# Kernel tuning notes

Measured on AMD Instinct MI355X. Metric: run time of the kernel, lower is better.

The kernel has to match this reference:

```python
import jax, jax.numpy as jnp
import numpy as np

E, B, T, DIN, D = 8, 16, 512, 256, 256  # ensemble, batch, seq, input_dim, d_model*factor


def setup_inputs() -> dict:
    key = jax.random.key(0)
    ks = jax.random.split(key, 9)
    s_in = 1.0 / np.sqrt(DIN)
    s_d = 1.0 / np.sqrt(D)
    return {
        "x": jax.random.normal(ks[0], (E, B, T, DIN), jnp.float32),
        "hidden": jnp.zeros((1, E * B, 2 * D), jnp.float32),
        "rnn_start": (jax.random.uniform(ks[1], (B, T, 1)) < 0.02).astype(jnp.float32),
        "W_in": jax.random.normal(ks[2], (2, E, DIN, D), jnp.float32) * s_in,
        "b_in": jax.random.normal(ks[3], (2, E, D), jnp.float32) * 0.01,
        "W_mid": jax.random.normal(ks[4], (4, E, D, D), jnp.float32) * s_d,
        "b_mid": jax.random.normal(ks[5], (4, E, D), jnp.float32) * 0.01,
        "W_out": jax.random.normal(ks[6], (E, D, D), jnp.float32) * s_d,
        "b_out": jax.random.normal(ks[7], (E, D), jnp.float32) * 0.01,
    }


def _scan_tie_input_gate(v, f, h0):
    # h_t = f_t * h_{t-1} + (1 - f_t) * v_t  (tied input gate), via associative scan.
    # v, f: [N, T, D]; h0: [N, 1, D]
    b = (1.0 - f) * v

    def combine(x, y):
        a1, b1 = x
        a2, b2 = y
        return a1 * a2, a2 * b1 + b2

    A, Bc = jax.lax.associative_scan(combine, (f, b), axis=1)
    out = A * h0 + Bc  # [N, T, D]
    return out, out[:, -1:, :]


def reference(x, hidden, rnn_start, W_in, b_in, W_mid, b_mid, W_out, b_out):
    # --- first GILR stage ---
    u = jnp.einsum('ebti,meio->mebto', x, W_in) + b_in[:, :, None, None, :]
    v = jnp.tanh(u[0])
    f = jax.nn.sigmoid(u[1])
    f = f * (1.0 - rnn_start)[None]  # rnn_start [B,T,1] broadcasts over E, D

    vr = v.reshape(E * B, T, D)
    fr = f.reshape(E * B, T, D)

    h_pre, h_mid = jnp.split(hidden, 2, axis=-1)          # each [1, E*B, D]
    h_pre = jnp.transpose(h_pre, (1, 0, 2))               # [E*B, 1, D]
    h_mid = jnp.transpose(h_mid, (1, 0, 2))

    vr, h_pre_last = _scan_tie_input_gate(vr, fr, h_pre)
    v4 = vr.reshape(E, B, T, D)

    # --- LSTM-like middle stage ---
    u = jnp.einsum('ebti,meio->mebto', v4, W_mid) + b_mid[:, :, None, None, :]
    f = jax.nn.sigmoid(u[0])
    i = jax.nn.sigmoid(u[1])
    o = jax.nn.sigmoid(u[2])
    z = jnp.tanh(u[3])
    f = f * (1.0 - rnn_start)[None]

    fr = f.reshape(E * B, T, D)
    izr = (i * z).reshape(E * B, T, D)
    orr = o.reshape(E * B, T, D)

    out, h_mid_last = _scan_tie_input_gate(izr, fr, h_mid)
    out = out * orr
    out4 = out.reshape(E, B, T, D)

    # --- output projection ---
    out4 = jnp.einsum('ebti,eio->ebto', out4, W_out) + b_out[:, None, None, :]

    hidden_out = jnp.transpose(jnp.concatenate([h_pre_last, h_mid_last], axis=-1), (1, 0, 2))
    return out4, hidden_out
```

## Files before the change

kernel.cpp:

```cpp
#include <hip/hip_runtime.h>
#include <hip/hip_bf16.h>
#include <stdint.h>
#include <stddef.h>


typedef __bf16 bf16x8 __attribute__((ext_vector_type(8)));
typedef __bf16 bf16x4 __attribute__((ext_vector_type(4)));
typedef __bf16 bf16x2 __attribute__((ext_vector_type(2)));
typedef float  f32x4  __attribute__((ext_vector_type(4)));
typedef unsigned int u32x2 __attribute__((ext_vector_type(2)));

#define E_ 8
#define M_ 8192
#define K_ 256

__device__ __forceinline__ float sigm_f(float x) {
    return __builtin_amdgcn_rcpf(1.0f + __expf(-x));
}
__device__ __forceinline__ float tanh_f(float x) {
    return 1.0f - 2.0f * __builtin_amdgcn_rcpf(1.0f + __expf(2.0f * x));
}

__device__ __forceinline__ void g2lds16(const void* g, void* l) {
    __builtin_amdgcn_global_load_lds((const __attribute__((address_space(1))) void*)g,
                                     (__attribute__((address_space(3))) void*)l, 16, 0, 0);
}

template <int D>
__device__ __forceinline__ float dppshr(float x) {
    return __builtin_bit_cast(float,
        __builtin_amdgcn_update_dpp(0, __builtin_bit_cast(int, x),
                                    0x110 | D, 0xF, 0xF, true));
}

__device__ __forceinline__ void lane_scan(float& A, float& B, float& EA, float& EB, int ln15) {
    float As, Bs;
    Bs = dppshr<1>(B); As = dppshr<1>(A); B = __builtin_fmaf(A, Bs, B); A = (ln15 >= 1) ? A * As : A;
    Bs = dppshr<2>(B); As = dppshr<2>(A); B = __builtin_fmaf(A, Bs, B); A = (ln15 >= 2) ? A * As : A;
    Bs = dppshr<4>(B); As = dppshr<4>(A); B = __builtin_fmaf(A, Bs, B); A = (ln15 >= 4) ? A * As : A;
    Bs = dppshr<8>(B); As = dppshr<8>(A); B = __builtin_fmaf(A, Bs, B); A = (ln15 >= 8) ? A * As : A;
    EA = dppshr<1>(A); EA = (ln15 >= 1) ? EA : 1.0f;
    EB = dppshr<1>(B);
}

__global__ __launch_bounds__(256) void convx_k(const float* __restrict__ x, __bf16* __restrict__ xb) {
    int i = blockIdx.x * 256 + threadIdx.x;
    float4 v = ((const float4*)x)[i];
    bf16x4 o;
    o[0] = (__bf16)v.x; o[1] = (__bf16)v.y; o[2] = (__bf16)v.z; o[3] = (__bf16)v.w;
    ((bf16x4*)xb)[i] = o;
}

__global__ __launch_bounds__(256) void transw_k(const float* __restrict__ src, __bf16* __restrict__ dst,
                                                int NG, int ilv) {
    int ge = blockIdx.z;
    int g = ge >> 3, e = ge & 7;
    int k0 = blockIdx.x * 64, d0 = blockIdx.y * 64;
    __shared__ float tile[64][65];
    int t = threadIdx.x;
#pragma unroll
    for (int j = 0; j < 16; ++j) {
        int lin = j * 256 + t;
        int r = lin >> 6, c = lin & 63;
        tile[r][c] = src[((size_t)(ge * 256 + k0 + r)) * 256 + d0 + c];
    }
    __syncthreads();
#pragma unroll
    for (int j = 0; j < 16; ++j) {
        int lin = j * 256 + t;
        int r = lin >> 6, c = lin & 63;
        int d = d0 + r;
        int row = ilv ? (d * NG + g) : (g * 256 + d);
        dst[((size_t)(e * NG * 256 + row)) * K_ + k0 + c] = (__bf16)tile[c][r];
    }
}

template <int MODE, int NG>
__global__ __launch_bounds__(512, 1) void gemm_k(const __bf16* __restrict__ A,
                                                 const __bf16* __restrict__ Wt,
                                                 const float* __restrict__ bias,
                                                 const float* __restrict__ rs,
                                                 __bf16* __restrict__ gout,
                                                 float* __restrict__ fout,
                                                 const float* __restrict__ hidden,
                                                 float* __restrict__ hidout) {
    constexpr int NT  = NG * 2;
    constexpr int NMT = 2 * NT;
    const int tid = threadIdx.x;
    const int bid = blockIdx.x;
    const int e  = bid & 7;
    const int rr = bid >> 3;
    const int nt = rr & (NT - 1);
    const int ms = rr / NT;
    const int mt0 = ms * NMT;
    const int lane = tid & 63, wid = tid >> 6;
    const int wr = wid >> 2, wc = wid & 3;
    const int ln15 = lane & 15, ln16 = lane >> 4;

    __shared__ __align__(16) __bf16 As[2][32768];
    __shared__ float cAl[64], cBl[64];
    __shared__ float chL[2][64];

    bf16x8 Breg[2][8];
    {
        const __bf16* bp = Wt + ((size_t)e * (NG * 256) + nt * 128 + wc * 32 + ln15) * K_ + ln16 * 8;
#pragma unroll
        for (int j = 0; j < 2; ++j)
#pragma unroll
            for (int s = 0; s < 8; ++s)
                Breg[j][s] = *(const bf16x8*)(bp + (size_t)j * 16 * K_ + s * 32);
    }
    f32x4 bias_v[2];
#pragma unroll
    for (int j = 0; j < 2; ++j) {
        int n0 = nt * 128 + wc * 32 + j * 16 + (ln16 << 2);
        if constexpr (MODE == 0) {
#pragma unroll
            for (int q = 0; q < 4; ++q) {
                int n = n0 + q;
                bias_v[j][q] = bias[((n & 1) * E_ + e) * 256 + (n >> 1)];
            }
        } else if constexpr (MODE == 1) {
#pragma unroll
            for (int q = 0; q < 4; ++q) {
                int n = n0 + q;
                bias_v[j][q] = bias[((n & 3) * E_ + e) * 256 + (n >> 2)];
            }
        } else {
            bias_v[j] = *(const f32x4*)&bias[e * 256 + n0];
        }
    }

    const size_t Ae = ((size_t)e * M_ + (size_t)mt0 * 128) * K_;
    const int sr = tid >> 5, sr2 = sr >> 2;
    const int gg0 = (tid & 31) ^ sr2;
    const __bf16* sE = A + Ae + (size_t)sr * K_ + gg0 * 8;
    const __bf16* sO = A + Ae + (size_t)sr * K_ + (gg0 ^ 4) * 8;
    __bf16* const dbase0 = &As[0][tid * 8];
    __bf16* const dbase1 = &As[1][tid * 8];

    auto stage = [&](int tt, int buf) {
        __bf16* d = buf ? dbase1 : dbase0;
        const size_t toff = (size_t)tt * (128 * K_);
#pragma unroll
        for (int q = 0; q < 8; ++q)
            g2lds16(((q & 1) ? sO : sE) + toff + q * (16 * K_), d + q * 4096);
    };

    const int rowb = (wr * 64 + ln15 * 4) * K_;
    const int gb = ln16 ^ (lane & 7);
    const int pe_off = rowb + gb * 8;
    const int po_off = rowb + (gb ^ 4) * 8;

    f32x4 acc[4][2] = {};

    auto compute = [&](int buf) {
        const __bf16* pe = &As[0][0] + buf * 32768 + pe_off;
        const __bf16* po = &As[0][0] + buf * 32768 + po_off;
#pragma unroll
        for (int s = 0; s < 8; ++s) {
            const __bf16* p = (s & 1) ? po : pe;
            bf16x8 af[4];
#pragma unroll
            for (int i = 0; i < 4; ++i)
                af[i] = *(const bf16x8*)(p + i * K_ + (s >> 1) * 64);
#pragma unroll
            for (int i = 0; i < 4; ++i)
#pragma unroll
                for (int j = 0; j < 2; ++j)
                    acc[i][j] = __builtin_amdgcn_mfma_f32_16x16x32_bf16(Breg[j][s], af[i], acc[i][j], 0, 0, 0);
        }
    };

    stage(0, 0);
    asm volatile("s_waitcnt vmcnt(0)" ::: "memory");
    __builtin_amdgcn_s_barrier();
    __builtin_amdgcn_sched_barrier(0);

    int buf = 0;
    for (int t = 0; t < NMT; ++t) {
        if (t + 1 < NMT) stage(t + 1, buf ^ 1);
        compute(buf);

        const int mt = mt0 + t;
        const int mb = mt * 128 + wr * 64 + ln15 * 4;

        if constexpr (MODE == 2) {
#pragma unroll
            for (int j = 0; j < 2; ++j) {
                const int n0 = nt * 128 + wc * 32 + j * 16 + (ln16 << 2);
#pragma unroll
                for (int i = 0; i < 4; ++i) {
                    f32x4 o = acc[i][j] + bias_v[j];
                    *(f32x4*)&fout[((size_t)e * M_ + mb + i) * 256 + n0] = o;
                    acc[i][j] = f32x4{};
                }
            }
        } else {
            f32x4 rs4 = *(const f32x4*)&rs[mb];
            f32x4 rsv;
#pragma unroll
            for (int q = 0; q < 4; ++q) rsv[q] = 1.0f - rs4[q];
            const bool cs = ((t & 3) == 0);
            const int c = t >> 2;

            if constexpr (MODE == 1) {
                float PA[2][4], PB[2][4], Ov[2][4], LA[2], LB[2], EA[2], EB[2];
#pragma unroll
                for (int j = 0; j < 2; ++j) {
#pragma unroll
                    for (int i = 0; i < 4; ++i) {
                        float f  = sigm_f(acc[i][j][0] + bias_v[j][0]) * rsv[i];
                        float iv = sigm_f(acc[i][j][1] + bias_v[j][1]);
                        float o  = sigm_f(acc[i][j][2] + bias_v[j][2]);
                        float z  = tanh_f(acc[i][j][3] + bias_v[j][3]);
                        float b  = (1.0f - f) * iv * z;
                        Ov[j][i] = o;
                        if (i == 0) { PA[j][0] = f; PB[j][0] = b; }
                        else { PB[j][i] = __builtin_fmaf(f, PB[j][i - 1], b); PA[j][i] = PA[j][i - 1] * f; }
                        acc[i][j] = f32x4{};
                    }
                    LA[j] = PA[j][3]; LB[j] = PB[j][3];
                    lane_scan(LA[j], LB[j], EA[j], EB[j], ln15);
                }
                if (wr == 0 && ln15 == 15) {
#pragma unroll
                    for (int j = 0; j < 2; ++j) {
                        int sl = wc * 8 + j * 4 + ln16;
                        cAl[sl] = LA[j]; cBl[sl] = LB[j];
                    }
                }
                asm volatile("s_waitcnt lgkmcnt(0)" ::: "memory");
                __builtin_amdgcn_s_barrier();
#pragma unroll
                for (int j = 0; j < 2; ++j) {
                    const int sl = wc * 8 + j * 4 + ln16;
                    const int d = nt * 32 + wc * 8 + j * 4 + ln16;
                    float hp = cs ? hidden[(e * 16 + ms * 4 + c) * 512 + 256 + d]
                                  : chL[t & 1][sl];
                    float hs = wr ? __builtin_fmaf(cAl[sl], hp, cBl[sl]) : hp;
                    float h0 = __builtin_fmaf(EA[j], hs, EB[j]);
#pragma unroll
                    for (int i = 0; i < 4; ++i) {
                        float h = __builtin_fmaf(PA[j][i], h0, PB[j][i]);
                        gout[((size_t)e * M_ + mb + i) * 256 + d] = (__bf16)(h * Ov[j][i]);
                    }
                    if (wr == 1 && ln15 == 15) {
                        float he = __builtin_fmaf(LA[j], hs, LB[j]);
                        chL[(t + 1) & 1][sl] = he;
                        if ((t & 3) == 3)
                            hidout[(e * 16 + ms * 4 + c) * 512 + 256 + d] = he;
                    }
                }
            } else {
                float PA[2][2][4], PB[2][2][4], LA[2][2], LB[2][2], EA[2][2], EB[2][2];
#pragma unroll
                for (int j = 0; j < 2; ++j) {
#pragma unroll
                    for (int dq = 0; dq < 2; ++dq) {
#pragma unroll
                        for (int i = 0; i < 4; ++i) {
                            float uv = acc[i][j][dq * 2 + 0] + bias_v[j][dq * 2 + 0];
                            float uf = acc[i][j][dq * 2 + 1] + bias_v[j][dq * 2 + 1];
                            float f = sigm_f(uf) * rsv[i];
                            float b = (1.0f - f) * tanh_f(uv);
                            if (i == 0) { PA[j][dq][0] = f; PB[j][dq][0] = b; }
                            else { PB[j][dq][i] = __builtin_fmaf(f, PB[j][dq][i - 1], b);
                                   PA[j][dq][i] = PA[j][dq][i - 1] * f; }
                        }
                        LA[j][dq] = PA[j][dq][3]; LB[j][dq] = PB[j][dq][3];
                        lane_scan(LA[j][dq], LB[j][dq], EA[j][dq], EB[j][dq], ln15);
                    }
#pragma unroll
                    for (int i = 0; i < 4; ++i) acc[i][j] = f32x4{};
                }
                if (wr == 0 && ln15 == 15) {
#pragma unroll
                    for (int j = 0; j < 2; ++j)
#pragma unroll
                        for (int dq = 0; dq < 2; ++dq) {
                            int sl = wc * 16 + j * 8 + ln16 * 2 + dq;
                            cAl[sl] = LA[j][dq]; cBl[sl] = LB[j][dq];
                        }
                }
                asm volatile("s_waitcnt lgkmcnt(0)" ::: "memory");
                __builtin_amdgcn_s_barrier();
#pragma unroll
                for (int j = 0; j < 2; ++j) {
                    const int D0 = nt * 64 + wc * 16 + j * 8 + ln16 * 2;
                    float h0q[2];
#pragma unroll
                    for (int dq = 0; dq < 2; ++dq) {
                        const int sl = wc * 16 + j * 8 + ln16 * 2 + dq;
                        float hp = cs ? hidden[(e * 16 + ms * 2 + c) * 512 + D0 + dq]
                                      : chL[t & 1][sl];
                        float hs = wr ? __builtin_fmaf(cAl[sl], hp, cBl[sl]) : hp;
                        h0q[dq] = __builtin_fmaf(EA[j][dq], hs, EB[j][dq]);
                        if (wr == 1 && ln15 == 15) {
                            float he = __builtin_fmaf(LA[j][dq], hs, LB[j][dq]);
                            chL[(t + 1) & 1][sl] = he;
                            if ((t & 3) == 3)
                                hidout[(e * 16 + ms * 2 + c) * 512 + D0 + dq] = he;
                        }
                    }
#pragma unroll
                    for (int i = 0; i < 4; ++i) {
                        float ha = __builtin_fmaf(PA[j][0][i], h0q[0], PB[j][0][i]);
                        float hb = __builtin_fmaf(PA[j][1][i], h0q[1], PB[j][1][i]);
                        bf16x2 pk; pk[0] = (__bf16)ha; pk[1] = (__bf16)hb;
                        *(unsigned int*)&gout[((size_t)e * M_ + mb + i) * 256 + D0] =
                            __builtin_bit_cast(unsigned int, pk);
                    }
                }
            }
        }
        asm volatile("s_waitcnt vmcnt(8) lgkmcnt(0)" ::: "memory");
        __builtin_amdgcn_s_barrier();
        __builtin_amdgcn_sched_barrier(0);
        buf ^= 1;
    }
}

extern "C" void kernel_launch(void* const* d_in, const int* in_sizes, int n_in,
                              void* d_out, int out_size, void* d_ws, size_t ws_size,
                              hipStream_t stream) {
    const float* x      = (const float*)d_in[0];
    const float* hidden = (const float*)d_in[1];
    const float* rs     = (const float*)d_in[2];
    const float* W_in   = (const float*)d_in[3];
    const float* b_in   = (const float*)d_in[4];
    const float* W_mid  = (const float*)d_in[5];
    const float* b_mid  = (const float*)d_in[6];
    const float* W_out  = (const float*)d_in[7];
    const float* b_out  = (const float*)d_in[8];
    float* out = (float*)d_out;

    char* ws = (char*)d_ws;
    const size_t MiB = (size_t)1 << 20;
    __bf16* Wt1 = (__bf16*)(ws + 0);
    __bf16* Wt2 = (__bf16*)(ws + 2 * MiB);
    __bf16* Wt3 = (__bf16*)(ws + 6 * MiB);
    __bf16* v4b = (__bf16*)(ws + 8 * MiB);
    __bf16* xb  = (__bf16*)(ws + 40 * MiB);
    __bf16* G   = (__bf16*)(ws + 72 * MiB);

    float* hidout = out + (size_t)E_ * M_ * 256;

    convx_k<<<16384, 256, 0, stream>>>(x, xb);
    transw_k<<<dim3(4, 4, 16), 256, 0, stream>>>(W_in, Wt1, 2, 1);
    transw_k<<<dim3(4, 4, 32), 256, 0, stream>>>(W_mid, Wt2, 4, 1);
    transw_k<<<dim3(4, 4, 8), 256, 0, stream>>>(W_out, Wt3, 1, 0);

    gemm_k<0, 2><<<256, 512, 0, stream>>>(xb, Wt1, b_in, rs, v4b, nullptr, hidden, hidout);
    gemm_k<1, 4><<<256, 512, 0, stream>>>(v4b, Wt2, b_mid, rs, G, nullptr, hidden, hidout);
    gemm_k<2, 1><<<256, 512, 0, stream>>>(G, Wt3, b_out, nullptr, nullptr, out, nullptr, nullptr);
}
```

Measured before the change: 179.5 us.

## Halve per-block M range and split K into LDS halves for more blocks

```diff
diff --git a/kernel.cpp b/kernel.cpp
--- a/kernel.cpp
+++ b/kernel.cpp
@@ -76,7 +76,7 @@
 }
 
 template <int MODE, int NG>
-__global__ __launch_bounds__(512, 1) void gemm_k(const __bf16* __restrict__ A,
+__global__ __launch_bounds__(512, 4) void gemm_k(const __bf16* __restrict__ A,
                                                  const __bf16* __restrict__ Wt,
                                                  const float* __restrict__ bias,
                                                  const float* __restrict__ rs,
@@ -85,7 +85,8 @@
                                                  const float* __restrict__ hidden,
                                                  float* __restrict__ hidout) {
     constexpr int NT  = NG * 2;
-    constexpr int NMT = 2 * NT;
+    constexpr int NMT = NT;
+    constexpr int CH  = (NT >> 2) ? (NT >> 2) : 1;
     const int tid = threadIdx.x;
     const int bid = blockIdx.x;
     const int e  = bid & 7;
@@ -97,7 +98,7 @@
     const int wr = wid >> 2, wc = wid & 3;
     const int ln15 = lane & 15, ln16 = lane >> 4;
 
-    __shared__ __align__(16) __bf16 As[2][32768];
+    __shared__ __align__(16) __bf16 As[2][16384];
     __shared__ float cAl[64], cBl[64];
     __shared__ float chL[2][64];
 
@@ -132,55 +133,66 @@
     }
 
     const size_t Ae = ((size_t)e * M_ + (size_t)mt0 * 128) * K_;
-    const int sr = tid >> 5, sr2 = sr >> 2;
-    const int gg0 = (tid & 31) ^ sr2;
-    const __bf16* sE = A + Ae + (size_t)sr * K_ + gg0 * 8;
-    const __bf16* sO = A + Ae + (size_t)sr * K_ + (gg0 ^ 4) * 8;
-    __bf16* const dbase0 = &As[0][tid * 8];
-    __bf16* const dbase1 = &As[1][tid * 8];
-
-    auto stage = [&](int tt, int buf) {
-        __bf16* d = buf ? dbase1 : dbase0;
-        const size_t toff = (size_t)tt * (128 * K_);
-#pragma unroll
-        for (int q = 0; q < 8; ++q)
-            g2lds16(((q & 1) ? sO : sE) + toff + q * (16 * K_), d + q * 4096);
+    const int tr = tid >> 4;
+    const int g16 = tid & 15;
+    __bf16* const db0 = &As[0][tid * 8];
+    __bf16* const db1 = &As[1][tid * 8];
+
+    auto stage = [&](int tt, int kc, int buf) {
+        const __bf16* sA = A + Ae + (size_t)tt * (128 * K_) + kc * 128;
+        __bf16* d = buf ? db1 : db0;
+#pragma unroll
+        for (int q = 0; q < 4; ++q) {
+            int row = q * 32 + tr;
+            int key = (row >> 2) & 7;
+            g2lds16(sA + (size_t)row * K_ + ((g16 ^ key) * 8), d + q * 4096);
+        }
     };
 
-    const int rowb = (wr * 64 + ln15 * 4) * K_;
-    const int gb = ln16 ^ (lane & 7);
-    const int pe_off = rowb + gb * 8;
-    const int po_off = rowb + (gb ^ 4) * 8;
+    const int row0 = wr * 64 + ln15 * 4;
+    const int kb = ((ln15 >> 2) & 1) * 32;
+    const int b0 = ln16 ^ (ln15 & 3);
+    const int pe_off = row0 * 128 + kb + b0 * 8;
+    const int po_off = row0 * 128 + (32 - kb) + b0 * 8;
 
     f32x4 acc[4][2] = {};
 
-    auto compute = [&](int buf) {
-        const __bf16* pe = &As[0][0] + buf * 32768 + pe_off;
-        const __bf16* po = &As[0][0] + buf * 32768 + po_off;
-#pragma unroll
-        for (int s = 0; s < 8; ++s) {
-            const __bf16* p = (s & 1) ? po : pe;
+    auto compute = [&](int buf, int kc) {
+        const __bf16* pe = &As[0][0] + buf * 16384 + pe_off;
+        const __bf16* po = &As[0][0] + buf * 16384 + po_off;
+#pragma unroll
+        for (int ks = 0; ks < 4; ++ks) {
+            const __bf16* p = (ks & 1) ? po : pe;
             bf16x8 af[4];
 #pragma unroll
             for (int i = 0; i < 4; ++i)
-                af[i] = *(const bf16x8*)(p + i * K_ + (s >> 1) * 64);
+                af[i] = *(const bf16x8*)(p + i * 128 + (ks >> 1) * 64);
 #pragma unroll
             for (int i = 0; i < 4; ++i)
 #pragma unroll
                 for (int j = 0; j < 2; ++j)
-                    acc[i][j] = __builtin_amdgcn_mfma_f32_16x16x32_bf16(Breg[j][s], af[i], acc[i][j], 0, 0, 0);
+                    acc[i][j] = __builtin_amdgcn_mfma_f32_16x16x32_bf16(Breg[j][kc * 4 + ks], af[i], acc[i][j], 0, 0, 0);
         }
     };
 
-    stage(0, 0);
+    stage(0, 0, 0);
     asm volatile("s_waitcnt vmcnt(0)" ::: "memory");
     __builtin_amdgcn_s_barrier();
     __builtin_amdgcn_sched_barrier(0);
 
-    int buf = 0;
     for (int t = 0; t < NMT; ++t) {
-        if (t + 1 < NMT) stage(t + 1, buf ^ 1);
-        compute(buf);
+        const bool pf = (t + 1 < NMT);
+        stage(t, 1, 1);
+        compute(0, 0);
+        __builtin_amdgcn_s_barrier();
+        if (pf) {
+            stage(t + 1, 0, 0);
+            asm volatile("s_waitcnt vmcnt(4)" ::: "memory");
+        } else {
+            asm volatile("s_waitcnt vmcnt(0)" ::: "memory");
+        }
+        __builtin_amdgcn_s_barrier();
+        compute(1, 1);
 
         const int mt = mt0 + t;
         const int mb = mt * 128 + wr * 64 + ln15 * 4;
@@ -203,6 +215,7 @@
             for (int q = 0; q < 4; ++q) rsv[q] = 1.0f - rs4[q];
             const bool cs = ((t & 3) == 0);
             const int c = t >> 2;
+            const int nrow = e * 16 + ms * CH + c;
 
             if constexpr (MODE == 1) {
                 float PA[2][4], PB[2][4], Ov[2][4], LA[2], LB[2], EA[2], EB[2];
@@ -236,8 +249,7 @@
                 for (int j = 0; j < 2; ++j) {
                     const int sl = wc * 8 + j * 4 + ln16;
                     const int d = nt * 32 + wc * 8 + j * 4 + ln16;
-                    float hp = cs ? hidden[(e * 16 + ms * 4 + c) * 512 + 256 + d]
-                                  : chL[t & 1][sl];
+                    float hp = cs ? hidden[nrow * 512 + 256 + d] : chL[t & 1][sl];
                     float hs = wr ? __builtin_fmaf(cAl[sl], hp, cBl[sl]) : hp;
                     float h0 = __builtin_fmaf(EA[j], hs, EB[j]);
 #pragma unroll
@@ -249,7 +261,7 @@
                         float he = __builtin_fmaf(LA[j], hs, LB[j]);
                         chL[(t + 1) & 1][sl] = he;
                         if ((t & 3) == 3)
-                            hidout[(e * 16 + ms * 4 + c) * 512 + 256 + d] = he;
+                            hidout[nrow * 512 + 256 + d] = he;
                     }
                 }
             } else {
@@ -292,15 +304,14 @@
 #pragma unroll
                     for (int dq = 0; dq < 2; ++dq) {
                         const int sl = wc * 16 + j * 8 + ln16 * 2 + dq;
-                        float hp = cs ? hidden[(e * 16 + ms * 2 + c) * 512 + D0 + dq]
-                                      : chL[t & 1][sl];
+                        float hp = cs ? hidden[nrow * 512 + D0 + dq] : chL[t & 1][sl];
                         float hs = wr ? __builtin_fmaf(cAl[sl], hp, cBl[sl]) : hp;
                         h0q[dq] = __builtin_fmaf(EA[j][dq], hs, EB[j][dq]);
                         if (wr == 1 && ln15 == 15) {
                             float he = __builtin_fmaf(LA[j][dq], hs, LB[j][dq]);
                             chL[(t + 1) & 1][sl] = he;
                             if ((t & 3) == 3)
-                                hidout[(e * 16 + ms * 2 + c) * 512 + D0 + dq] = he;
+                                hidout[nrow * 512 + D0 + dq] = he;
                         }
                     }
 #pragma unroll
@@ -314,10 +325,10 @@
                 }
             }
         }
-        asm volatile("s_waitcnt vmcnt(8) lgkmcnt(0)" ::: "memory");
+        if (pf) asm volatile("s_waitcnt vmcnt(8) lgkmcnt(0)" ::: "memory");
+        else    asm volatile("s_waitcnt lgkmcnt(0)" ::: "memory");
         __builtin_amdgcn_s_barrier();
         __builtin_amdgcn_sched_barrier(0);
-        buf ^= 1;
     }
 }
 
@@ -351,7 +362,7 @@
     transw_k<<<dim3(4, 4, 32), 256, 0, stream>>>(W_mid, Wt2, 4, 1);
     transw_k<<<dim3(4, 4, 8), 256, 0, stream>>>(W_out, Wt3, 1, 0);
 
-    gemm_k<0, 2><<<256, 512, 0, stream>>>(xb, Wt1, b_in, rs, v4b, nullptr, hidden, hidout);
-    gemm_k<1, 4><<<256, 512, 0, stream>>>(v4b, Wt2, b_mid, rs, G, nullptr, hidden, hidout);
-    gemm_k<2, 1><<<256, 512, 0, stream>>>(G, Wt3, b_out, nullptr, nullptr, out, nullptr, nullptr);
-}
+    gemm_k<0, 2><<<512, 512, 0, stream>>>(xb, Wt1, b_in, rs, v4b, nullptr, hidden, hidout);
+    gemm_k<1, 4><<<512, 512, 0, stream>>>(v4b, Wt2, b_mid, rs, G, nullptr, hidden, hidout);
+    gemm_k<2, 1><<<512, 512, 0, stream>>>(G, Wt3, b_out, nullptr, nullptr, out, nullptr, nullptr);
+}
```

After: 200.3 us. +11.6%, slower.
